# Kernel tuning notes

Measured on AMD Instinct MI355X. Metric: run time of the kernel, lower is better.

## Reference

```python
import jax, jax.numpy as jnp
import numpy as np

EPS = 1e-6
ROPE_THETA = 1000000.0
SPAN_LENGTHS = [700, 300, 600, 448]
L, D, H, HK, DH, FF = 2, 2048, 16, 8, 128, 8192


def _rmsnorm(x, w):
    var = jnp.mean(jnp.square(x), axis=-1, keepdims=True)
    return x * jax.lax.rsqrt(var + EPS) * w


def _rotate_half(x):
    x1, x2 = jnp.split(x, 2, axis=-1)
    return jnp.concatenate([-x2, x1], axis=-1)


def setup_inputs() -> dict:
    key = jax.random.key(0)
    ks = jax.random.split(key, 8)
    s = 0.02  # init scale
    seg = np.repeat(np.arange(len(SPAN_LENGTHS), dtype=np.int32), SPAN_LENGTHS)
    pos = np.concatenate([np.arange(n, dtype=np.int32) for n in SPAN_LENGTHS])
    T = seg.shape[0]
    return {
        "hidden_states": jax.random.normal(ks[0], (T, D), jnp.float32),
        "ln1_w": jnp.ones((L, D), jnp.float32),
        "ln2_w": jnp.ones((L, D), jnp.float32),
        "wq": jax.random.normal(ks[1], (L, D, H * DH), jnp.float32) * s,
        "wk": jax.random.normal(ks[2], (L, D, HK * DH), jnp.float32) * s,
        "wv": jax.random.normal(ks[3], (L, D, HK * DH), jnp.float32) * s,
        "wo": jax.random.normal(ks[4], (L, H * DH, D), jnp.float32) * s,
        "qn_w": jnp.ones((L, DH), jnp.float32),
        "kn_w": jnp.ones((L, DH), jnp.float32),
        "wg": jax.random.normal(ks[5], (L, D, FF), jnp.float32) * s,
        "wu": jax.random.normal(ks[6], (L, D, FF), jnp.float32) * s,
        "wd": jax.random.normal(ks[7], (L, FF, D), jnp.float32) * s,
        "final_norm_w": jnp.ones((D,), jnp.float32),
        "segment_ids": jnp.asarray(seg),
        "position_ids": jnp.asarray(pos),
    }


def reference(hidden_states, ln1_w, ln2_w, wq, wk, wv, wo, qn_w, kn_w, wg, wu, wd, final_norm_w, segment_ids, position_ids):
    T = hidden_states.shape[0]
    # rotary tables from per-request positions (positions reset per span)
    inv_freq = 1.0 / (ROPE_THETA ** (jnp.arange(0, DH, 2, dtype=jnp.float32) / DH))
    freqs = position_ids.astype(jnp.float32)[:, None] * inv_freq  # [T, DH/2]
    emb = jnp.concatenate([freqs, freqs], axis=-1)                # [T, DH]
    cos = jnp.cos(emb)[:, None, :]
    sin = jnp.sin(emb)[:, None, :]
    # ragged causal mask: attend only within the same request span, causally
    tok = jnp.arange(T)
    mask = (segment_ids[:, None] == segment_ids[None, :]) & (tok[:, None] >= tok[None, :])
    neg = jnp.finfo(hidden_states.dtype).min
    scale = 1.0 / np.sqrt(DH)

    x = hidden_states
    for l in range(L):
        h = _rmsnorm(x, ln1_w[l])
        q = (h @ wq[l]).reshape(T, H, DH)
        k = (h @ wk[l]).reshape(T, HK, DH)
        v = (h @ wv[l]).reshape(T, HK, DH)
        q = _rmsnorm(q, qn_w[l])  # Qwen3 per-head q/k RMSNorm
        k = _rmsnorm(k, kn_w[l])
        q = q * cos + _rotate_half(q) * sin
        k = k * cos + _rotate_half(k) * sin
        rep = H // HK  # GQA
        k = jnp.repeat(k, rep, axis=1)
        v = jnp.repeat(v, rep, axis=1)
        scores = jnp.einsum('thd,shd->hts', q, k) * scale  # [H, T, T]
        scores = jnp.where(mask[None], scores, neg)
        attn = jax.nn.softmax(scores, axis=-1)
        o = jnp.einsum('hts,shd->thd', attn, v).reshape(T, H * DH)
        x = x + o @ wo[l]
        h = _rmsnorm(x, ln2_w[l])
        x = x + (jax.nn.silu(h @ wg[l]) * (h @ wu[l])) @ wd[l]
    return _rmsnorm(x, final_norm_w)
```

## Files before the change

### kernel.cpp

```cpp
#include <hip/hip_runtime.h>
#include <stdint.h>

#define T_SEQ 2048
#define DMODEL 2048
#define NH 16
#define NKV 8
#define DHEAD 128
#define DFF 8192

typedef float f32x4 __attribute__((ext_vector_type(4)));
typedef float f32x2 __attribute__((ext_vector_type(2)));
typedef __bf16 bf16x8 __attribute__((ext_vector_type(8)));
typedef unsigned short ushort_t;

typedef __attribute__((address_space(1))) void gvoid;
typedef __attribute__((address_space(3))) void lvoid;

__device__ inline unsigned short f2bf(float f) {
  unsigned int u = __float_as_uint(f);
  u += 0x7fffu + ((u >> 16) & 1u);
  return (unsigned short)(u >> 16);
}
__device__ inline float bf2f(unsigned short h) {
  return __uint_as_float(((unsigned int)h) << 16);
}

__device__ inline void gload_lds16(const void* g, void* l) {
  __builtin_amdgcn_global_load_lds((gvoid*)g, (lvoid*)l, 16, 0, 0);
}

template <typename TIN>
__global__ __launch_bounds__(256) void k_transpose_bf16(const TIN* __restrict__ in,
                                                        ushort_t* __restrict__ out,
                                                        int R, int C) {
  __shared__ float tile[64 * 72];
  int tid = threadIdx.x;
  int r0 = blockIdx.y * 64, c0 = blockIdx.x * 64;
  int rl = tid >> 4;
  int cc = tid & 15;
#pragma unroll
  for (int i = 0; i < 4; ++i) {
    int row = rl + i * 16;
    const TIN* src = in + (size_t)(r0 + row) * C + c0 + cc * 4;
    float v0, v1, v2, v3;
    if constexpr (sizeof(TIN) == 4) {
      f32x4 v = *(const f32x4*)src;
      v0 = v.x; v1 = v.y; v2 = v.z; v3 = v.w;
    } else {
      ushort4 v = *(const ushort4*)src;
      v0 = bf2f(v.x); v1 = bf2f(v.y); v2 = bf2f(v.z); v3 = bf2f(v.w);
    }
    int chunk = cc ^ (row & 15);
    f32x4 t = {v0, v1, v2, v3};
    *(f32x4*)&tile[row * 72 + chunk * 4] = t;
  }
  __syncthreads();
#pragma unroll
  for (int i = 0; i < 4; ++i) {
    int nrow = rl + i * 16;
    int k4 = cc * 4;
    ushort4 o;
    {
      int k = k4 + 0;
      o.x = f2bf(tile[k * 72 + (((nrow >> 2) ^ (k & 15)) << 2) + (nrow & 3)]);
      k = k4 + 1;
      o.y = f2bf(tile[k * 72 + (((nrow >> 2) ^ (k & 15)) << 2) + (nrow & 3)]);
      k = k4 + 2;
      o.z = f2bf(tile[k * 72 + (((nrow >> 2) ^ (k & 15)) << 2) + (nrow & 3)]);
      k = k4 + 3;
      o.w = f2bf(tile[k * 72 + (((nrow >> 2) ^ (k & 15)) << 2) + (nrow & 3)]);
    }
    *(ushort4*)(out + (size_t)(c0 + nrow) * R + r0 + k4) = o;
  }
}

template <int BF16OUT>
__global__ __launch_bounds__(256) void k_rmsnorm(const float* __restrict__ X,
                                                 const float* __restrict__ W,
                                                 void* __restrict__ OUT) {
  int row = blockIdx.x, tid = threadIdx.x;
  const float* xr = X + (size_t)row * DMODEL;
  f32x4 x0 = *(const f32x4*)(xr + tid * 4);
  f32x4 x1 = *(const f32x4*)(xr + 1024 + tid * 4);
  float ss = x0.x * x0.x + x0.y * x0.y + x0.z * x0.z + x0.w * x0.w +
             x1.x * x1.x + x1.y * x1.y + x1.z * x1.z + x1.w * x1.w;
#pragma unroll
  for (int o = 1; o < 64; o <<= 1) ss += __shfl_xor(ss, o, 64);
  __shared__ float red[4];
  int w = tid >> 6;
  if ((tid & 63) == 0) red[w] = ss;
  __syncthreads();
  float tot = red[0] + red[1] + red[2] + red[3];
  float sc = rsqrtf(tot / (float)DMODEL + 1e-6f);
  f32x4 w0 = *(const f32x4*)(W + tid * 4);
  f32x4 w1 = *(const f32x4*)(W + 1024 + tid * 4);
  if constexpr (BF16OUT) {
    ushort_t* o = (ushort_t*)OUT + (size_t)row * DMODEL;
    ushort4 a, b;
    a.x = f2bf(x0.x * sc * w0.x); a.y = f2bf(x0.y * sc * w0.y);
    a.z = f2bf(x0.z * sc * w0.z); a.w = f2bf(x0.w * sc * w0.w);
    b.x = f2bf(x1.x * sc * w1.x); b.y = f2bf(x1.y * sc * w1.y);
    b.z = f2bf(x1.z * sc * w1.z); b.w = f2bf(x1.w * sc * w1.w);
    *(ushort4*)(o + tid * 4) = a;
    *(ushort4*)(o + 1024 + tid * 4) = b;
  } else {
    float* o = (float*)OUT + (size_t)row * DMODEL;
    f32x4 a = {x0.x * sc * w0.x, x0.y * sc * w0.y, x0.z * sc * w0.z, x0.w * sc * w0.w};
    f32x4 b = {x1.x * sc * w1.x, x1.y * sc * w1.y, x1.z * sc * w1.z, x1.w * sc * w1.w};
    *(f32x4*)(o + tid * 4) = a;
    *(f32x4*)(o + 1024 + tid * 4) = b;
  }
}

template <int NZ, int WRITEH>
__global__ __launch_bounds__(512) void k_redln(const ushort_t* __restrict__ P,
                                               const float* __restrict__ RES,
                                               const float* __restrict__ W,
                                               float* __restrict__ OUT,
                                               ushort_t* __restrict__ HB) {
  int row = blockIdx.x, tid = threadIdx.x;
  size_t base = (size_t)row * DMODEL + tid * 4;
  f32x4 v = *(const f32x4*)(RES + base);
#pragma unroll
  for (int z = 0; z < NZ; ++z) {
    ushort4 t = *(const ushort4*)(P + (size_t)z * T_SEQ * DMODEL + base);
    v.x += bf2f(t.x); v.y += bf2f(t.y); v.z += bf2f(t.z); v.w += bf2f(t.w);
  }
  *(f32x4*)(OUT + base) = v;
  if constexpr (WRITEH) {
    float ss = v.x * v.x + v.y * v.y + v.z * v.z + v.w * v.w;
#pragma unroll
    for (int o = 1; o < 64; o <<= 1) ss += __shfl_xor(ss, o, 64);
    __shared__ float red[8];
    if ((tid & 63) == 0) red[tid >> 6] = ss;
    __syncthreads();
    float tot = 0.f;
#pragma unroll
    for (int i = 0; i < 8; ++i) tot += red[i];
    float sc = rsqrtf(tot / (float)DMODEL + 1e-6f);
    f32x4 wv = *(const f32x4*)(W + tid * 4);
    ushort4 h;
    h.x = f2bf(v.x * sc * wv.x); h.y = f2bf(v.y * sc * wv.y);
    h.z = f2bf(v.z * sc * wv.z); h.w = f2bf(v.w * sc * wv.w);
    *(ushort4*)(HB + base) = h;
  }
}

#define EPI_SILU 2
#define EPI_STOREB 3

#define LOAD_B256(bs, rbase)                                                   \
  {                                                                            \
    _Pragma("unroll") for (int ks = 0; ks < 2; ++ks)                           \
        _Pragma("unroll") for (int ni = 0; ni < 2; ++ni)                       \
            bfr[ks][ni] = *(const bf16x8*)((bs) +                              \
                (((rbase) + ni * 16 + lr) << 6) +                              \
                ((((ks << 2) + lg) ^ (lr & 7)) << 3));                         \
  }

#define MFMA_Q256(q)                                                           \
  {                                                                            \
    _Pragma("unroll") for (int ks = 0; ks < 2; ++ks)                           \
        _Pragma("unroll") for (int mi = 0; mi < 4; ++mi)                       \
            _Pragma("unroll") for (int ni = 0; ni < 2; ++ni)                   \
                acc[mi][(q) * 2 + ni] =                                        \
                    __builtin_amdgcn_mfma_f32_16x16x32_bf16(                   \
                        af[ks][mi], bfr[ks][ni], acc[mi][(q) * 2 + ni], 0, 0, 0); \
  }

template <int LAST>
__device__ __forceinline__ void g256_iter(
    const ushort_t* __restrict__ as, const ushort_t* __restrict__ bsA,
    const ushort_t* __restrict__ bsB, ushort_t* __restrict__ nA,
    ushort_t* __restrict__ nB, const ushort_t* __restrict__ an,
    const ushort_t* __restrict__ bn, size_t rs, int slds, int lr, int lg,
    f32x4 (&acc)[4][8]) {
  bf16x8 af[2][4], bfr[2][2];
#pragma unroll
  for (int ks = 0; ks < 2; ++ks)
#pragma unroll
    for (int mi = 0; mi < 4; ++mi)
      af[ks][mi] = *(const bf16x8*)(as + ((mi * 16 + lr) << 6) +
                                    ((((ks << 2) + lg) ^ (lr & 7)) << 3));
  LOAD_B256(bsA, 0);
  if constexpr (!LAST) {
    gload_lds16(an, nA + slds);
    gload_lds16(an + rs, nA + 4096 + slds);
  }
  __builtin_amdgcn_s_barrier();
  asm volatile("s_waitcnt lgkmcnt(0)" ::: "memory");
  __builtin_amdgcn_sched_barrier(0);
  __builtin_amdgcn_s_setprio(1);
  MFMA_Q256(0);
  __builtin_amdgcn_s_setprio(0);
  __builtin_amdgcn_s_barrier();
  LOAD_B256(bsA, 32);
  if constexpr (!LAST) {
    gload_lds16(an + 2 * rs, nA + 8192 + slds);
    gload_lds16(an + 3 * rs, nA + 12288 + slds);
    asm volatile("s_waitcnt vmcnt(4)" ::: "memory");
  } else {
    asm volatile("s_waitcnt vmcnt(0)" ::: "memory");
  }
  __builtin_amdgcn_s_barrier();
  asm volatile("s_waitcnt lgkmcnt(0)" ::: "memory");
  __builtin_amdgcn_sched_barrier(0);
  __builtin_amdgcn_s_setprio(1);
  MFMA_Q256(1);
  __builtin_amdgcn_s_setprio(0);
  __builtin_amdgcn_s_barrier();
  LOAD_B256(bsB, 0);
  if constexpr (!LAST) {
    gload_lds16(bn, nB + slds);
    gload_lds16(bn + 2 * rs, nB + 8192 + slds);
  }
  __builtin_amdgcn_s_barrier();
  asm volatile("s_waitcnt lgkmcnt(0)" ::: "memory");
  __builtin_amdgcn_sched_barrier(0);
  __builtin_amdgcn_s_setprio(1);
  MFMA_Q256(2);
  __builtin_amdgcn_s_setprio(0);
  __builtin_amdgcn_s_barrier();
  LOAD_B256(bsB, 32);
  if constexpr (!LAST) {
    gload_lds16(bn + rs, nB + 4096 + slds);
    gload_lds16(bn + 3 * rs, nB + 12288 + slds);
    asm volatile("s_waitcnt vmcnt(2)" ::: "memory");
  }
  __builtin_amdgcn_s_barrier();
  asm volatile("s_waitcnt lgkmcnt(0)" ::: "memory");
  __builtin_amdgcn_sched_barrier(0);
  __builtin_amdgcn_s_setprio(1);
  MFMA_Q256(3);
  __builtin_amdgcn_s_setprio(0);
  __builtin_amdgcn_s_barrier();
}

template <int EPI>
__global__ __launch_bounds__(512, 2) void k_gemm256(
    const ushort_t* __restrict__ A, const ushort_t* __restrict__ BT,
    const ushort_t* __restrict__ GINB, ushort_t* __restrict__ CB,
    int N, int Kstride, int Kc, size_t zoff) {
  __shared__ ushort_t lds[65536];
  const int tid = threadIdx.x;
  const int l = tid & 63, wid = tid >> 6;
  const int wm = wid >> 1, wn = wid & 1;
  const int lr = l & 15, lg = l >> 4;
  const int m0 = blockIdx.y * 256, n0 = blockIdx.x * 256;
  const int z = blockIdx.z;
  const int NT = Kc >> 6;

  A += (size_t)z * Kc;
  BT += (size_t)z * Kc;
  CB += (size_t)z * zoff;

  const int srow = tid >> 3;
  const int scs = (tid & 7) ^ (srow & 7);
  const size_t sgoff = (size_t)srow * Kstride + scs * 8;
  const int slds = wid * 512;

  const ushort_t* ga = A + (size_t)m0 * Kstride + sgoff;
  const ushort_t* gb = BT + (size_t)n0 * Kstride + sgoff;
  const size_t rs = (size_t)64 * Kstride;

  f32x4 acc[4][8] = {};

  ushort_t* Ab0 = lds;
  ushort_t* Bb0 = lds + 16384;
  ushort_t* Ab1 = lds + 32768;
  ushort_t* Bb1 = lds + 49152;

  gload_lds16(ga, Ab0 + slds);
  gload_lds16(ga + rs, Ab0 + 4096 + slds);
  gload_lds16(ga + 2 * rs, Ab0 + 8192 + slds);
  gload_lds16(ga + 3 * rs, Ab0 + 12288 + slds);
  gload_lds16(gb, Bb0 + slds);
  gload_lds16(gb + 2 * rs, Bb0 + 8192 + slds);
  gload_lds16(gb + rs, Bb0 + 4096 + slds);
  gload_lds16(gb + 3 * rs, Bb0 + 12288 + slds);
  asm volatile("s_waitcnt vmcnt(2)" ::: "memory");
  __builtin_amdgcn_s_barrier();

  for (int kt = 0; kt < NT - 1; ++kt) {
    const int d = kt & 1;
    const ushort_t* as = (d ? Ab1 : Ab0) + wm * 4096;
    const ushort_t* bsA = (d ? Bb1 : Bb0) + (wn * 2) * 4096;
    ushort_t* nA = d ? Ab0 : Ab1;
    ushort_t* nB = d ? Bb0 : Bb1;
    g256_iter<0>(as, bsA, bsA + 4096, nA, nB, ga + (size_t)(kt + 1) * 64,
                 gb + (size_t)(kt + 1) * 64, rs, slds, lr, lg, acc);
  }
  {
    const int d = (NT - 1) & 1;
    const ushort_t* as = (d ? Ab1 : Ab0) + wm * 4096;
    const ushort_t* bsA = (d ? Bb1 : Bb0) + (wn * 2) * 4096;
    g256_iter<1>(as, bsA, bsA + 4096, nullptr, nullptr, nullptr, nullptr, rs,
                 slds, lr, lg, acc);
  }

#pragma unroll
  for (int mi = 0; mi < 4; ++mi)
#pragma unroll
    for (int ci = 0; ci < 8; ++ci)
#pragma unroll
      for (int rr = 0; rr < 4; ++rr) {
        int m = m0 + wm * 64 + mi * 16 + lg * 4 + rr;
        int n = n0 + wn * 128 + ci * 16 + lr;
        size_t off = (size_t)m * N + n;
        float v = acc[mi][ci][rr];
        if constexpr (EPI == EPI_STOREB) {
          CB[off] = f2bf(v);
        } else {
          float gv = bf2f(GINB[off]);
          float s = gv / (1.f + __expf(-gv));
          CB[off] = f2bf(s * v);
        }
      }
}

__global__ __launch_bounds__(256) void k_qkv_post(const ushort_t* __restrict__ Q0,
                                                  const ushort_t* __restrict__ Q1,
                                                  const float* __restrict__ QNW,
                                                  const float* __restrict__ KNW,
                                                  const int* __restrict__ POS,
                                                  ushort_t* __restrict__ Qb,
                                                  ushort_t* __restrict__ Kb,
                                                  ushort_t* __restrict__ Vb) {
  int t = blockIdx.x;
  int tid = threadIdx.x;
  int w = tid >> 6, l = tid & 63;
  float pos = (float)POS[t];
  const ushort_t* base0 = Q0 + (size_t)t * 4096;
  const ushort_t* base1 = Q1 + (size_t)t * 4096;
  int i0 = 2 * (l & 31);
  const float K2 = 19.931568569324174f / 64.f;
  float ang0 = pos * exp2f(-(float)i0 * K2);
  float ang1 = pos * exp2f(-(float)(i0 + 1) * K2);
  float cs0 = cosf(ang0), sn0 = sinf(ang0);
  float cs1 = cosf(ang1), sn1 = sinf(ang1);
#pragma unroll
  for (int si = 0; si < 8; ++si) {
    int slot = w + si * 4;
    ushort2 xa = *(const ushort2*)(base0 + slot * 128 + l * 2);
    ushort2 xb = *(const ushort2*)(base1 + slot * 128 + l * 2);
    float v0 = bf2f(xa.x) + bf2f(xb.x), v1 = bf2f(xa.y) + bf2f(xb.y);
    float ss = v0 * v0 + v1 * v1;
#pragma unroll
    for (int o = 1; o < 64; o <<= 1) ss += __shfl_xor(ss, o, 64);
    if (slot < 24) {
      float sc = rsqrtf(ss / 128.f + 1e-6f);
      const float* wn = (slot < 16) ? QNW : KNW;
      f32x2 wv = *(const f32x2*)(wn + l * 2);
      v0 = v0 * sc * wv.x;
      v1 = v1 * sc * wv.y;
      float p0 = __shfl_xor(v0, 32, 64);
      float p1 = __shfl_xor(v1, 32, 64);
      float r0 = (l < 32) ? -p0 : p0;
      float r1 = (l < 32) ? -p1 : p1;
      v0 = v0 * cs0 + r0 * sn0;
      v1 = v1 * cs1 + r1 * sn1;
    }
    ushort2 uv;
    uv.x = f2bf(v0);
    uv.y = f2bf(v1);
    ushort_t* dst;
    if (slot < 16)
      dst = Qb + (size_t)t * 2048 + slot * 128 + l * 2;
    else if (slot < 24)
      dst = Kb + (size_t)t * 1024 + (slot - 16) * 128 + l * 2;
    else
      dst = Vb + (size_t)t * 1024 + (slot - 24) * 128 + l * 2;
    *(ushort2*)dst = uv;
  }
}

__global__ __launch_bounds__(64) void k_flash(const ushort_t* __restrict__ Qb,
                                              const ushort_t* __restrict__ Kb,
                                              const ushort_t* __restrict__ VT,
                                              const int* __restrict__ SEG,
                                              ushort_t* __restrict__ Ob) {
  __shared__ ushort_t Pl[2][16 * 40];
  int l = threadIdx.x;
  int qt = blockIdx.x, kvh = blockIdx.y;
  int q0 = qt * 16;
  int lr = l & 15, lg = l >> 4;
  int h0 = kvh * 2;
  bf16x8 qf0[4], qf1[4];
  {
    const bf16x8* qv = (const bf16x8*)(Qb + (size_t)(q0 + lr) * 2048 + h0 * 128);
#pragma unroll
    for (int kk = 0; kk < 4; ++kk) {
      qf0[kk] = qv[kk * 4 + lg];
      qf1[kk] = qv[16 + kk * 4 + lg];
    }
  }
  int segq[4];
#pragma unroll
  for (int r = 0; r < 4; ++r) segq[r] = SEG[q0 + lg * 4 + r];
  int target = SEG[q0];
  int lo = 0, hi = q0;
  while (lo < hi) {
    int mid = (lo + hi) >> 1;
    if (SEG[mid] < target) lo = mid + 1; else hi = mid;
  }
  int s_start = lo & ~31;
  float mr[2][4], lrun[2][4];
  f32x4 acc[2][8] = {};
#pragma unroll
  for (int h = 0; h < 2; ++h)
#pragma unroll
    for (int r = 0; r < 4; ++r) { mr[h][r] = -1e30f; lrun[h][r] = 0.f; }
  const float scale = 0.08838834764831845f;
  for (int s0 = s_start; s0 < q0 + 16; s0 += 32) {
    int sa = s0 + lr, sb = s0 + 16 + lr;
    int sac = min(sa, T_SEQ - 1), sbc = min(sb, T_SEQ - 1);
    bf16x8 vfr[8];
    int sbase = min(s0 + lg * 8, T_SEQ - 8);
#pragma unroll
    for (int c = 0; c < 8; ++c)
      vfr[c] = *(const bf16x8*)(VT + (size_t)(kvh * 128 + c * 16 + lr) * T_SEQ + sbase);
    f32x4 SA0 = {}, SB0 = {}, SA1 = {}, SB1 = {};
    const bf16x8* ka = (const bf16x8*)(Kb + (size_t)sac * 1024 + kvh * 128);
    const bf16x8* kb_ = (const bf16x8*)(Kb + (size_t)sbc * 1024 + kvh * 128);
#pragma unroll
    for (int kk = 0; kk < 4; ++kk) {
      bf16x8 kaf = ka[kk * 4 + lg];
      bf16x8 kbf = kb_[kk * 4 + lg];
      SA0 = __builtin_amdgcn_mfma_f32_16x16x32_bf16(qf0[kk], kaf, SA0, 0, 0, 0);
      SB0 = __builtin_amdgcn_mfma_f32_16x16x32_bf16(qf0[kk], kbf, SB0, 0, 0, 0);
      SA1 = __builtin_amdgcn_mfma_f32_16x16x32_bf16(qf1[kk], kaf, SA1, 0, 0, 0);
      SB1 = __builtin_amdgcn_mfma_f32_16x16x32_bf16(qf1[kk], kbf, SB1, 0, 0, 0);
    }
    int sga = SEG[sac], sgb = SEG[sbc];
    bool mAv[4], mBv[4];
#pragma unroll
    for (int r = 0; r < 4; ++r) {
      int qrow = q0 + lg * 4 + r;
      mAv[r] = (sa <= qrow) && (sga == segq[r]);
      mBv[r] = (sb <= qrow) && (sgb == segq[r]);
    }
#pragma unroll
    for (int h = 0; h < 2; ++h) {
#pragma unroll
      for (int r = 0; r < 4; ++r) {
        float sva = (h ? SA1[r] : SA0[r]);
        float svb = (h ? SB1[r] : SB0[r]);
        float xa = mAv[r] ? sva * scale : -1e30f;
        float xb = mBv[r] ? svb * scale : -1e30f;
        float mx = fmaxf(xa, xb);
#pragma unroll
        for (int o = 1; o < 16; o <<= 1) mx = fmaxf(mx, __shfl_xor(mx, o, 64));
        float nm = fmaxf(mr[h][r], mx);
        float ea = __expf(xa - nm), eb = __expf(xb - nm);
        float rsum = ea + eb;
#pragma unroll
        for (int o = 1; o < 16; o <<= 1) rsum += __shfl_xor(rsum, o, 64);
        float al = __expf(mr[h][r] - nm);
        lrun[h][r] = lrun[h][r] * al + rsum;
        mr[h][r] = nm;
#pragma unroll
        for (int c = 0; c < 8; ++c) acc[h][c][r] *= al;
        Pl[h][(lg * 4 + r) * 40 + lr] = f2bf(ea);
        Pl[h][(lg * 4 + r) * 40 + 16 + lr] = f2bf(eb);
      }
    }
    asm volatile("s_waitcnt lgkmcnt(0)" ::: "memory");
    bf16x8 pa0 = *(const bf16x8*)&Pl[0][lr * 40 + lg * 8];
    bf16x8 pa1 = *(const bf16x8*)&Pl[1][lr * 40 + lg * 8];
#pragma unroll
    for (int c = 0; c < 8; ++c) {
      acc[0][c] = __builtin_amdgcn_mfma_f32_16x16x32_bf16(pa0, vfr[c], acc[0][c], 0, 0, 0);
      acc[1][c] = __builtin_amdgcn_mfma_f32_16x16x32_bf16(pa1, vfr[c], acc[1][c], 0, 0, 0);
    }
  }
#pragma unroll
  for (int h = 0; h < 2; ++h)
#pragma unroll
    for (int c = 0; c < 8; ++c)
#pragma unroll
      for (int r = 0; r < 4; ++r) {
        float ov = acc[h][c][r] / lrun[h][r];
        Ob[(size_t)(q0 + lg * 4 + r) * 2048 + (h0 + h) * 128 + c * 16 + lr] = f2bf(ov);
      }
}

extern "C" void kernel_launch(void* const* d_in, const int* in_sizes, int n_in,
                              void* d_out, int out_size, void* d_ws, size_t ws_size,
                              hipStream_t stream) {
  const float* hidden = (const float*)d_in[0];
  const float* ln1 = (const float*)d_in[1];
  const float* ln2 = (const float*)d_in[2];
  const float* wq = (const float*)d_in[3];
  const float* wk = (const float*)d_in[4];
  const float* wv = (const float*)d_in[5];
  const float* wo = (const float*)d_in[6];
  const float* qnw = (const float*)d_in[7];
  const float* knw = (const float*)d_in[8];
  const float* wg = (const float*)d_in[9];
  const float* wu = (const float*)d_in[10];
  const float* wd = (const float*)d_in[11];
  const float* fnw = (const float*)d_in[12];
  const int* seg = (const int*)d_in[13];
  const int* pos = (const int*)d_in[14];
  float* out = (float*)d_out;

  char* ws = (char*)d_ws;
  size_t off = 0;
  auto alloc = [&](size_t bytes) {
    char* p = ws + off;
    off += (bytes + 255) & ~(size_t)255;
    return p;
  };
  ushort_t* wT = (ushort_t*)alloc((size_t)DFF * DMODEL * 2);
  ushort_t* hbuf = (ushort_t*)alloc((size_t)T_SEQ * DMODEL * 2);
  ushort_t* qb = (ushort_t*)alloc((size_t)T_SEQ * 2048 * 2);
  ushort_t* kb = (ushort_t*)alloc((size_t)T_SEQ * 1024 * 2);
  ushort_t* vb = (ushort_t*)alloc((size_t)T_SEQ * 1024 * 2);
  ushort_t* vT = (ushort_t*)alloc((size_t)T_SEQ * 1024 * 2);
  ushort_t* ob = (ushort_t*)alloc((size_t)T_SEQ * 2048 * 2);
  ushort_t* qkvp = (ushort_t*)alloc((size_t)2 * T_SEQ * 4096 * 2);
  ushort_t* pbuf = (ushort_t*)alloc((size_t)4 * T_SEQ * DMODEL * 2);
  ushort_t* gbufB = (ushort_t*)alloc((size_t)T_SEQ * DFF * 2);
  ushort_t* mbuf = (ushort_t*)alloc((size_t)T_SEQ * DFF * 2);
  (void)ws_size; (void)in_sizes; (void)n_in; (void)out_size;

  dim3 b256(256), b64(64), b512(512);
  k_rmsnorm<1><<<T_SEQ, b256, 0, stream>>>(hidden, ln1, hbuf);

  for (int lyr = 0; lyr < 2; ++lyr) {
    const float* xsrc = (lyr == 0) ? hidden : out;

    const float* wql = wq + (size_t)lyr * DMODEL * 2048;
    const float* wkl = wk + (size_t)lyr * DMODEL * 1024;
    const float* wvl = wv + (size_t)lyr * DMODEL * 1024;
    k_transpose_bf16<float><<<dim3(32, 32), b256, 0, stream>>>(wql, wT, 2048, 2048);
    k_transpose_bf16<float><<<dim3(16, 32), b256, 0, stream>>>(wkl, wT + (size_t)2048 * 2048, 2048, 1024);
    k_transpose_bf16<float><<<dim3(16, 32), b256, 0, stream>>>(wvl, wT + (size_t)3072 * 2048, 2048, 1024);
    k_gemm256<EPI_STOREB><<<dim3(16, 8, 2), b512, 0, stream>>>(
        hbuf, wT, nullptr, qkvp, 4096, 2048, 1024, (size_t)2048 * 4096);
    k_qkv_post<<<T_SEQ, b256, 0, stream>>>(qkvp, qkvp + (size_t)2048 * 4096,
                                           qnw + (size_t)lyr * 128, knw + (size_t)lyr * 128,
                                           pos, qb, kb, vb);
    k_transpose_bf16<ushort_t><<<dim3(16, 32), b256, 0, stream>>>(vb, vT, 2048, 1024);
    k_flash<<<dim3(T_SEQ / 16, NKV), b64, 0, stream>>>(qb, kb, vT, seg, ob);

    const float* wol = wo + (size_t)lyr * 2048 * DMODEL;
    k_transpose_bf16<float><<<dim3(32, 32), b256, 0, stream>>>(wol, wT, 2048, 2048);
    k_gemm256<EPI_STOREB><<<dim3(8, 8, 4), b512, 0, stream>>>(
        ob, wT, nullptr, pbuf, 2048, 2048, 512, (size_t)2048 * 2048);
    k_redln<4, 1><<<T_SEQ, b512, 0, stream>>>(pbuf, xsrc,
                                              ln2 + (size_t)lyr * DMODEL, out, hbuf);

    const float* wgl = wg + (size_t)lyr * DMODEL * DFF;
    const float* wul = wu + (size_t)lyr * DMODEL * DFF;
    const float* wdl = wd + (size_t)lyr * DFF * DMODEL;
    k_transpose_bf16<float><<<dim3(128, 32), b256, 0, stream>>>(wgl, wT, 2048, 8192);
    k_gemm256<EPI_STOREB><<<dim3(32, 8, 1), b512, 0, stream>>>(
        hbuf, wT, nullptr, gbufB, 8192, 2048, 2048, 0);
    k_transpose_bf16<float><<<dim3(128, 32), b256, 0, stream>>>(wul, wT, 2048, 8192);
    k_gemm256<EPI_SILU><<<dim3(32, 8, 1), b512, 0, stream>>>(
        hbuf, wT, gbufB, mbuf, 8192, 2048, 2048, 0);
    k_transpose_bf16<float><<<dim3(32, 128), b256, 0, stream>>>(wdl, wT, 8192, 2048);
    k_gemm256<EPI_STOREB><<<dim3(8, 8, 4), b512, 0, stream>>>(
        mbuf, wT, nullptr, pbuf, 2048, 8192, 2048, (size_t)2048 * 2048);
    if (lyr == 0) {
      k_redln<4, 1><<<T_SEQ, b512, 0, stream>>>(pbuf, out, ln1 + DMODEL, out, hbuf);
    } else {
      k_redln<4, 0><<<T_SEQ, b512, 0, stream>>>(pbuf, out, nullptr, out, nullptr);
    }
  }
  k_rmsnorm<0><<<T_SEQ, b256, 0, stream>>>(out, fnw, out);
}
```

Measured before the change: 893.8 us.

## Fuse gate and up projections into one interleaved GEMM with GLU epilogue

Gate and up weights are transposed into one interleaved B matrix (alternating 16-row blocks), so a single GEMM computes both projections and applies silu(g)*u in its epilogue. This drops the gate intermediate buffer's write and read and one GEMM launch. The main loop also issues all next-tile B loads earlier and removes several barriers to deepen overlap. Block IDs are remapped into grouped chunks for better L2 reuse. The barrier removal carries a risk of LDS races, and the swizzle assumes grid dimensions divide evenly.

Result: faster. 830.9 us (-7.0%).

```diff
diff --git a/kernel.cpp b/kernel.cpp
--- a/kernel.cpp
+++ b/kernel.cpp
@@ -32,7 +32,7 @@
 template <typename TIN>
 __global__ __launch_bounds__(256) void k_transpose_bf16(const TIN* __restrict__ in,
                                                         ushort_t* __restrict__ out,
-                                                        int R, int C) {
+                                                        int R, int C, int rmode) {
   __shared__ float tile[64 * 72];
   int tid = threadIdx.x;
   int r0 = blockIdx.y * 64, c0 = blockIdx.x * 64;
@@ -70,7 +70,11 @@
       k = k4 + 3;
       o.w = f2bf(tile[k * 72 + (((nrow >> 2) ^ (k & 15)) << 2) + (nrow & 3)]);
     }
-    *(ushort4*)(out + (size_t)(c0 + nrow) * R + r0 + k4) = o;
+    int n = c0 + nrow;
+    int orow = n;
+    if (rmode == 1) orow = ((n >> 4) << 5) + (n & 15);
+    else if (rmode == 2) orow = ((n >> 4) << 5) + 16 + (n & 15);
+    *(ushort4*)(out + (size_t)orow * R + r0 + k4) = o;
   }
 }
 
@@ -146,8 +150,8 @@
   }
 }
 
-#define EPI_SILU 2
 #define EPI_STOREB 3
+#define EPI_GLU 5
 
 #define LOAD_B256(bs, rbase)                                                   \
   {                                                                            \
@@ -186,6 +190,8 @@
   if constexpr (!LAST) {
     gload_lds16(an, nA + slds);
     gload_lds16(an + rs, nA + 4096 + slds);
+    gload_lds16(bn, nB + slds);
+    gload_lds16(bn + 2 * rs, nB + 8192 + slds);
   }
   __builtin_amdgcn_s_barrier();
   asm volatile("s_waitcnt lgkmcnt(0)" ::: "memory");
@@ -193,12 +199,13 @@
   __builtin_amdgcn_s_setprio(1);
   MFMA_Q256(0);
   __builtin_amdgcn_s_setprio(0);
-  __builtin_amdgcn_s_barrier();
   LOAD_B256(bsA, 32);
   if constexpr (!LAST) {
     gload_lds16(an + 2 * rs, nA + 8192 + slds);
     gload_lds16(an + 3 * rs, nA + 12288 + slds);
-    asm volatile("s_waitcnt vmcnt(4)" ::: "memory");
+    gload_lds16(bn + rs, nB + 4096 + slds);
+    gload_lds16(bn + 3 * rs, nB + 12288 + slds);
+    asm volatile("s_waitcnt vmcnt(8)" ::: "memory");
   } else {
     asm volatile("s_waitcnt vmcnt(0)" ::: "memory");
   }
@@ -208,23 +215,15 @@
   __builtin_amdgcn_s_setprio(1);
   MFMA_Q256(1);
   __builtin_amdgcn_s_setprio(0);
-  __builtin_amdgcn_s_barrier();
   LOAD_B256(bsB, 0);
-  if constexpr (!LAST) {
-    gload_lds16(bn, nB + slds);
-    gload_lds16(bn + 2 * rs, nB + 8192 + slds);
-  }
   __builtin_amdgcn_s_barrier();
   asm volatile("s_waitcnt lgkmcnt(0)" ::: "memory");
   __builtin_amdgcn_sched_barrier(0);
   __builtin_amdgcn_s_setprio(1);
   MFMA_Q256(2);
   __builtin_amdgcn_s_setprio(0);
-  __builtin_amdgcn_s_barrier();
   LOAD_B256(bsB, 32);
   if constexpr (!LAST) {
-    gload_lds16(bn + rs, nB + 4096 + slds);
-    gload_lds16(bn + 3 * rs, nB + 12288 + slds);
     asm volatile("s_waitcnt vmcnt(2)" ::: "memory");
   }
   __builtin_amdgcn_s_barrier();
@@ -239,14 +238,22 @@
 template <int EPI>
 __global__ __launch_bounds__(512, 2) void k_gemm256(
     const ushort_t* __restrict__ A, const ushort_t* __restrict__ BT,
-    const ushort_t* __restrict__ GINB, ushort_t* __restrict__ CB,
-    int N, int Kstride, int Kc, size_t zoff) {
+    ushort_t* __restrict__ CB, int N, int Kstride, int Kc, size_t zoff) {
   __shared__ ushort_t lds[65536];
   const int tid = threadIdx.x;
   const int l = tid & 63, wid = tid >> 6;
   const int wm = wid >> 1, wn = wid & 1;
   const int lr = l & 15, lg = l >> 4;
-  const int m0 = blockIdx.y * 256, n0 = blockIdx.x * 256;
+  const int gx = gridDim.x;
+  const int nwg = gx * gridDim.y;
+  const int bid = blockIdx.x + gx * blockIdx.y;
+  const int chunk = nwg >> 3;
+  const int x = bid & 7;
+  const int local = bid >> 3;
+  const int cn = chunk >> 2;
+  const int ncx = gx / cn;
+  const int m0 = ((x / ncx) * 4 + local / cn) * 256;
+  const int n0 = ((x % ncx) * cn + local % cn) * 256;
   const int z = blockIdx.z;
   const int NT = Kc >> 6;
 
@@ -272,10 +279,10 @@
 
   gload_lds16(ga, Ab0 + slds);
   gload_lds16(ga + rs, Ab0 + 4096 + slds);
+  gload_lds16(gb, Bb0 + slds);
+  gload_lds16(gb + 2 * rs, Bb0 + 8192 + slds);
   gload_lds16(ga + 2 * rs, Ab0 + 8192 + slds);
   gload_lds16(ga + 3 * rs, Ab0 + 12288 + slds);
-  gload_lds16(gb, Bb0 + slds);
-  gload_lds16(gb + 2 * rs, Bb0 + 8192 + slds);
   gload_lds16(gb + rs, Bb0 + 4096 + slds);
   gload_lds16(gb + 3 * rs, Bb0 + 12288 + slds);
   asm volatile("s_waitcnt vmcnt(2)" ::: "memory");
@@ -298,24 +305,33 @@
                  slds, lr, lg, acc);
   }
 
-#pragma unroll
-  for (int mi = 0; mi < 4; ++mi)
-#pragma unroll
-    for (int ci = 0; ci < 8; ++ci)
-#pragma unroll
-      for (int rr = 0; rr < 4; ++rr) {
-        int m = m0 + wm * 64 + mi * 16 + lg * 4 + rr;
-        int n = n0 + wn * 128 + ci * 16 + lr;
-        size_t off = (size_t)m * N + n;
-        float v = acc[mi][ci][rr];
-        if constexpr (EPI == EPI_STOREB) {
-          CB[off] = f2bf(v);
-        } else {
-          float gv = bf2f(GINB[off]);
+  if constexpr (EPI == EPI_GLU) {
+#pragma unroll
+    for (int mi = 0; mi < 4; ++mi)
+#pragma unroll
+      for (int ci = 0; ci < 8; ci += 2)
+#pragma unroll
+        for (int rr = 0; rr < 4; ++rr) {
+          int m = m0 + wm * 64 + mi * 16 + lg * 4 + rr;
+          int nblk = n0 + wn * 128 + ci * 16;
+          int col = ((nblk >> 5) << 4) + lr;
+          float gv = acc[mi][ci][rr];
+          float uv = acc[mi][ci + 1][rr];
           float s = gv / (1.f + __expf(-gv));
-          CB[off] = f2bf(s * v);
+          CB[(size_t)m * 8192 + col] = f2bf(s * uv);
         }
-      }
+  } else {
+#pragma unroll
+    for (int mi = 0; mi < 4; ++mi)
+#pragma unroll
+      for (int ci = 0; ci < 8; ++ci)
+#pragma unroll
+        for (int rr = 0; rr < 4; ++rr) {
+          int m = m0 + wm * 64 + mi * 16 + lg * 4 + rr;
+          int n = n0 + wn * 128 + ci * 16 + lr;
+          CB[(size_t)m * N + n] = f2bf(acc[mi][ci][rr]);
+        }
+  }
 }
 
 __global__ __launch_bounds__(256) void k_qkv_post(const ushort_t* __restrict__ Q0,
@@ -511,7 +527,7 @@
     off += (bytes + 255) & ~(size_t)255;
     return p;
   };
-  ushort_t* wT = (ushort_t*)alloc((size_t)DFF * DMODEL * 2);
+  ushort_t* wT = (ushort_t*)alloc((size_t)2 * DFF * DMODEL * 2);
   ushort_t* hbuf = (ushort_t*)alloc((size_t)T_SEQ * DMODEL * 2);
   ushort_t* qb = (ushort_t*)alloc((size_t)T_SEQ * 2048 * 2);
   ushort_t* kb = (ushort_t*)alloc((size_t)T_SEQ * 1024 * 2);
@@ -520,7 +536,6 @@
   ushort_t* ob = (ushort_t*)alloc((size_t)T_SEQ * 2048 * 2);
   ushort_t* qkvp = (ushort_t*)alloc((size_t)2 * T_SEQ * 4096 * 2);
   ushort_t* pbuf = (ushort_t*)alloc((size_t)4 * T_SEQ * DMODEL * 2);
-  ushort_t* gbufB = (ushort_t*)alloc((size_t)T_SEQ * DFF * 2);
   ushort_t* mbuf = (ushort_t*)alloc((size_t)T_SEQ * DFF * 2);
   (void)ws_size; (void)in_sizes; (void)n_in; (void)out_size;
 
@@ -533,36 +548,34 @@
     const float* wql = wq + (size_t)lyr * DMODEL * 2048;
     const float* wkl = wk + (size_t)lyr * DMODEL * 1024;
     const float* wvl = wv + (size_t)lyr * DMODEL * 1024;
-    k_transpose_bf16<float><<<dim3(32, 32), b256, 0, stream>>>(wql, wT, 2048, 2048);
-    k_transpose_bf16<float><<<dim3(16, 32), b256, 0, stream>>>(wkl, wT + (size_t)2048 * 2048, 2048, 1024);
-    k_transpose_bf16<float><<<dim3(16, 32), b256, 0, stream>>>(wvl, wT + (size_t)3072 * 2048, 2048, 1024);
+    k_transpose_bf16<float><<<dim3(32, 32), b256, 0, stream>>>(wql, wT, 2048, 2048, 0);
+    k_transpose_bf16<float><<<dim3(16, 32), b256, 0, stream>>>(wkl, wT + (size_t)2048 * 2048, 2048, 1024, 0);
+    k_transpose_bf16<float><<<dim3(16, 32), b256, 0, stream>>>(wvl, wT + (size_t)3072 * 2048, 2048, 1024, 0);
     k_gemm256<EPI_STOREB><<<dim3(16, 8, 2), b512, 0, stream>>>(
-        hbuf, wT, nullptr, qkvp, 4096, 2048, 1024, (size_t)2048 * 4096);
+        hbuf, wT, qkvp, 4096, 2048, 1024, (size_t)2048 * 4096);
     k_qkv_post<<<T_SEQ, b256, 0, stream>>>(qkvp, qkvp + (size_t)2048 * 4096,
                                            qnw + (size_t)lyr * 128, knw + (size_t)lyr * 128,
                                            pos, qb, kb, vb);
-    k_transpose_bf16<ushort_t><<<dim3(16, 32), b256, 0, stream>>>(vb, vT, 2048, 1024);
+    k_transpose_bf16<ushort_t><<<dim3(16, 32), b256, 0, stream>>>(vb, vT, 2048, 1024, 0);
     k_flash<<<dim3(T_SEQ / 16, NKV), b64, 0, stream>>>(qb, kb, vT, seg, ob);
 
     const float* wol = wo + (size_t)lyr * 2048 * DMODEL;
-    k_transpose_bf16<float><<<dim3(32, 32), b256, 0, stream>>>(wol, wT, 2048, 2048);
+    k_transpose_bf16<float><<<dim3(32, 32), b256, 0, stream>>>(wol, wT, 2048, 2048, 0);
     k_gemm256<EPI_STOREB><<<dim3(8, 8, 4), b512, 0, stream>>>(
-        ob, wT, nullptr, pbuf, 2048, 2048, 512, (size_t)2048 * 2048);
+        ob, wT, pbuf, 2048, 2048, 512, (size_t)2048 * 2048);
     k_redln<4, 1><<<T_SEQ, b512, 0, stream>>>(pbuf, xsrc,
                                               ln2 + (size_t)lyr * DMODEL, out, hbuf);
 
     const float* wgl = wg + (size_t)lyr * DMODEL * DFF;
     const float* wul = wu + (size_t)lyr * DMODEL * DFF;
     const float* wdl = wd + (size_t)lyr * DFF * DMODEL;
-    k_transpose_bf16<float><<<dim3(128, 32), b256, 0, stream>>>(wgl, wT, 2048, 8192);
-    k_gemm256<EPI_STOREB><<<dim3(32, 8, 1), b512, 0, stream>>>(
-        hbuf, wT, nullptr, gbufB, 8192, 2048, 2048, 0);
-    k_transpose_bf16<float><<<dim3(128, 32), b256, 0, stream>>>(wul, wT, 2048, 8192);
-    k_gemm256<EPI_SILU><<<dim3(32, 8, 1), b512, 0, stream>>>(
-        hbuf, wT, gbufB, mbuf, 8192, 2048, 2048, 0);
-    k_transpose_bf16<float><<<dim3(32, 128), b256, 0, stream>>>(wdl, wT, 8192, 2048);
+    k_transpose_bf16<float><<<dim3(128, 32), b256, 0, stream>>>(wgl, wT, 2048, 8192, 1);
+    k_transpose_bf16<float><<<dim3(128, 32), b256, 0, stream>>>(wul, wT, 2048, 8192, 2);
+    k_gemm256<EPI_GLU><<<dim3(64, 8, 1), b512, 0, stream>>>(
+        hbuf, wT, mbuf, 16384, 2048, 2048, 0);
+    k_transpose_bf16<float><<<dim3(32, 128), b256, 0, stream>>>(wdl, wT, 8192, 2048, 0);
     k_gemm256<EPI_STOREB><<<dim3(8, 8, 4), b512, 0, stream>>>(
-        mbuf, wT, nullptr, pbuf, 2048, 8192, 2048, (size_t)2048 * 2048);
+        mbuf, wT, pbuf, 2048, 8192, 2048, (size_t)2048 * 2048);
     if (lyr == 0) {
       k_redln<4, 1><<<T_SEQ, b512, 0, stream>>>(pbuf, out, ln1 + DMODEL, out, hbuf);
     } else {
```
